# Performance work log

Hardware: AMD Instinct MI355X
Metric: run time of the kernel (lower is better)

Reference implementation:

```python
import jax, jax.numpy as jnp
import numpy as np

EXPR_MASK_RATIO = 0.4
POS_MASK_RATIO = 0.33
MIN_VISIBLE_GENES = 10


def setup_inputs() -> dict:
    key = jax.random.key(0)
    k1, k2 = jax.random.split(key)
    expression = jax.random.normal(k1, (16, 1024, 2000), dtype=jnp.float32)
    position = jax.random.normal(k2, (16, 1024, 3), dtype=jnp.float32)
    return {"expression": expression, "position": position}


def _expression_mask(expression, key):
    # strategy == 'random': rand matrix, kthvalue threshold, mask = rand >= threshold
    B, N, G = expression.shape
    num_masked = max(1, int(G * EXPR_MASK_RATIO))
    num_masked = min(num_masked, G - MIN_VISIBLE_GENES)
    rand = jax.random.uniform(key, (B, N, G), dtype=jnp.float32)
    # torch.kthvalue(rand, G - num_masked): (G - num_masked)-th smallest value,
    # i.e. index G - num_masked - 1 of the ascending sort (keepdim=True).
    kth = jnp.sort(rand, axis=-1)[..., G - num_masked - 1 : G - num_masked]  # (B,N,1)
    return rand >= kth  # bool (B,N,G); includes the threshold element, as in torch code


def _position_mask(position, key):
    # Vectorized form of the per-(b,n) loop:
    #   r < ratio*0.3      -> mask 2 of 3 dims (randperm(3)[:2] == complement of one uniform dim)
    #   ratio*0.3 <= r < ratio -> mask 1 uniform dim
    B, N, _ = position.shape
    kr, k1, k2 = jax.random.split(key, 3)
    r = jax.random.uniform(kr, (B, N), dtype=jnp.float32)
    two = r < POS_MASK_RATIO * 0.3
    one = (r < POS_MASK_RATIO) & (~two)
    dim1 = jax.random.randint(k1, (B, N), 0, 3)  # dim masked in the 1-dim branch
    excl = jax.random.randint(k2, (B, N), 0, 3)  # dim kept in the 2-dim branch
    eye = jnp.eye(3, dtype=bool)
    m1 = eye[dim1]        # (B,N,3) one-hot
    m2 = ~eye[excl]       # (B,N,3) two hot
    false3 = jnp.zeros((B, N, 3), dtype=bool)
    return jnp.where(two[..., None], m2, jnp.where(one[..., None], m1, false3))


def reference(expression, position):
    key = jax.random.key(42)
    ke, kp = jax.random.split(key)
    expr_mask = _expression_mask(expression, ke)   # (B,N,G) bool
    pos_mask = _position_mask(position, kp)        # (B,N,3) bool
    return expr_mask, pos_mask
```

## Files before the change

### kernel.cpp

```cpp
#include <hip/hip_runtime.h>
#include <stdint.h>

#define TF_ROUND(x0, x1, r)                    \
  {                                            \
    x0 += x1;                                  \
    x1 = (x1 << (r)) | (x1 >> (32 - (r)));     \
    x1 ^= x0;                                  \
  }

__host__ __device__ inline void threefry2x32(uint32_t k0, uint32_t k1,
                                             uint32_t x0, uint32_t x1,
                                             uint32_t& o0, uint32_t& o1) {
  const uint32_t ks2 = k0 ^ k1 ^ 0x1BD11BDAu;
  x0 += k0; x1 += k1;
  TF_ROUND(x0, x1, 13) TF_ROUND(x0, x1, 15) TF_ROUND(x0, x1, 26) TF_ROUND(x0, x1, 6)
  x0 += k1; x1 += ks2 + 1u;
  TF_ROUND(x0, x1, 17) TF_ROUND(x0, x1, 29) TF_ROUND(x0, x1, 16) TF_ROUND(x0, x1, 24)
  x0 += ks2; x1 += k0 + 2u;
  TF_ROUND(x0, x1, 13) TF_ROUND(x0, x1, 15) TF_ROUND(x0, x1, 26) TF_ROUND(x0, x1, 6)
  x0 += k0; x1 += k1 + 3u;
  TF_ROUND(x0, x1, 17) TF_ROUND(x0, x1, 29) TF_ROUND(x0, x1, 16) TF_ROUND(x0, x1, 24)
  x0 += k1; x1 += ks2 + 4u;
  TF_ROUND(x0, x1, 13) TF_ROUND(x0, x1, 15) TF_ROUND(x0, x1, 26) TF_ROUND(x0, x1, 6)
  x0 += ks2; x1 += k0 + 5u;
  o0 = x0; o1 = x1;
}

#define RND4(r)                                                     \
  _Pragma("unroll") for (int e = 0; e < 4; ++e) {                   \
    x0[e] += x1[e];                                                 \
    x1[e] = __builtin_amdgcn_alignbit(x1[e], x1[e], 32u - (r));     \
    x1[e] ^= x0[e];                                                 \
  }
#define INJ4(a, b)                                                  \
  _Pragma("unroll") for (int e = 0; e < 4; ++e) {                   \
    x0[e] += (a);                                                   \
    x1[e] += (b);                                                   \
  }

__device__ __forceinline__ void tf4(uint32_t k0, uint32_t k1, uint32_t ks2,
                                    uint32_t tbk, uint32_t lit, uint32_t out[4]) {
  uint32_t x0[4], x1[4];
#pragma unroll
  for (int e = 0; e < 4; ++e) { x0[e] = k0; x1[e] = tbk + (lit + (uint32_t)e); }
  RND4(13) RND4(15) RND4(26) RND4(6)
  INJ4(k1, ks2 + 1u)
  RND4(17) RND4(29) RND4(16) RND4(24)
  INJ4(ks2, k0 + 2u)
  RND4(13) RND4(15) RND4(26) RND4(6)
  INJ4(k0, k1 + 3u)
  RND4(17) RND4(29) RND4(16) RND4(24)
  INJ4(k1, ks2 + 4u)
  RND4(13) RND4(15) RND4(26) RND4(6)
#pragma unroll
  for (int e = 0; e < 4; ++e) out[e] = (x0[e] + ks2) ^ (x1[e] + (k0 + 5u));
}

constexpr int B = 16;
constexpr int N = 1024;
constexpr int G = 2000;
constexpr int NUM_ROWS = B * N;
constexpr uint32_t RANK = (uint32_t)(G - 800 - 1);
constexpr long long EXPR_ELEMS = (long long)NUM_ROWS * G;
constexpr int ROWS_PER_BLOCK = 4;

typedef int v4i __attribute__((ext_vector_type(4)));

__global__ __launch_bounds__(256) void fused_mask_kernel(
    int32_t* __restrict__ out_expr, int32_t* __restrict__ out_pos,
    uint32_t ke0, uint32_t ke1,
    uint32_t kr0, uint32_t kr1,
    uint32_t ah0, uint32_t ah1, uint32_t al0, uint32_t al1,
    uint32_t bh0, uint32_t bh1, uint32_t bl0, uint32_t bl1) {
  __shared__ alignas(16) uint32_t hist[ROWS_PER_BLOCK][256];
  __shared__ uint32_t cand[ROWS_PER_BLOCK][64];
  __shared__ uint32_t cnt[ROWS_PER_BLOCK];

  const int t = threadIdx.x;
  const int lane = t & 63;
  const int w = t >> 6;
  const uint32_t row = blockIdx.x * (uint32_t)ROWS_PER_BLOCK + (uint32_t)w;
  const uint32_t rbase = row * (uint32_t)G;

  {
    uint4 z = make_uint4(0u, 0u, 0u, 0u);
    *reinterpret_cast<uint4*>(&hist[w][lane * 4]) = z;
  }
  if (lane == 0) cnt[w] = 0u;
  __builtin_amdgcn_wave_barrier();

  const uint32_t ks2 = ke0 ^ ke1 ^ 0x1BD11BDAu;
  const uint32_t tbk = rbase + (uint32_t)(lane << 2) + ke1;

  uint32_t m[32];
  uint32_t pb = 0u;

#pragma unroll
  for (int j = 0; j < 7; ++j) {
    uint32_t o[4];
    tf4(ke0, ke1, ks2, tbk, (uint32_t)(j * 256), o);
#pragma unroll
    for (int e = 0; e < 4; ++e) {
      m[j * 4 + e] = o[e] >> 9;
      atomicAdd(&hist[w][o[e] >> 24], 1u);
    }
  }
  if (lane < 52) {
    uint32_t o[4];
    tf4(ke0, ke1, ks2, tbk, 1792u, o);
#pragma unroll
    for (int e = 0; e < 4; ++e) {
      m[28 + e] = o[e] >> 9;
      atomicAdd(&hist[w][o[e] >> 24], 1u);
    }
  } else {
#pragma unroll
    for (int e = 0; e < 4; ++e) m[28 + e] = 0xFFFFFFFFu;
    if (lane < 57) {
      uint32_t pk0, pk1;
      switch (lane) {
        case 52: pk0 = kr0; pk1 = kr1; break;
        case 53: pk0 = ah0; pk1 = ah1; break;
        case 54: pk0 = al0; pk1 = al1; break;
        case 55: pk0 = bh0; pk1 = bh1; break;
        default: pk0 = bl0; pk1 = bl1; break;
      }
      uint32_t y0, y1;
      threefry2x32(pk0, pk1, 0u, row, y0, y1);
      pb = y0 ^ y1;
    }
  }
  __builtin_amdgcn_wave_barrier();

  uint4 h = *reinterpret_cast<const uint4*>(&hist[w][lane * 4]);
  uint32_t tot = h.x + h.y + h.z + h.w;
  uint32_t x = tot;
#pragma unroll
  for (int d = 1; d < 64; d <<= 1) {
    uint32_t o = __shfl_up(x, d, 64);
    if (lane >= d) x += o;
  }
  const uint32_t e0 = x - tot;
  bool found = (e0 <= RANK) && (RANK < x);
  uint32_t bl_ = 0u, kl = 0u;
  if (found) {
    uint32_t e1 = e0 + h.x, e2 = e1 + h.y, e3 = e2 + h.z;
    if (RANK < e1)      { bl_ = 4u * lane + 0u; kl = RANK - e0; }
    else if (RANK < e2) { bl_ = 4u * lane + 1u; kl = RANK - e1; }
    else if (RANK < e3) { bl_ = 4u * lane + 2u; kl = RANK - e2; }
    else                { bl_ = 4u * lane + 3u; kl = RANK - e3; }
  }
  unsigned long long bm = __ballot(found);
  const int src = __builtin_ctzll(bm);
  const uint32_t bucket = (uint32_t)__shfl((int)bl_, src, 64);
  const uint32_t kk = (uint32_t)__shfl((int)kl, src, 64);

#pragma unroll
  for (int i = 0; i < 32; ++i) {
    if ((m[i] >> 15) == bucket) {
      uint32_t p = atomicAdd(&cnt[w], 1u);
      if (p < 64u) cand[w][p] = m[i];
    }
  }
  __builtin_amdgcn_wave_barrier();

  uint32_t c = cnt[w];
  c = (uint32_t)__builtin_amdgcn_readfirstlane((int)c);
  if (c > 64u) c = 64u;
  uint32_t myc = cand[w][lane];
  uint32_t r = 0u;
  for (uint32_t j = 0; j < c; ++j) {
    uint32_t vj = (uint32_t)__shfl((int)myc, (int)j, 64);
    r += (vj < myc || (vj == myc && j < (uint32_t)lane)) ? 1u : 0u;
  }
  bool win = ((uint32_t)lane < c) && (r == kk);
  unsigned long long wm = __ballot(win);
  const uint32_t thr = (uint32_t)__shfl((int)myc, __builtin_ctzll(wm), 64);

  {
    uint32_t p0 = (uint32_t)__shfl((int)pb, 52, 64);
    uint32_t p1 = (uint32_t)__shfl((int)pb, 53, 64);
    uint32_t p2 = (uint32_t)__shfl((int)pb, 54, 64);
    uint32_t p3 = (uint32_t)__shfl((int)pb, 55, 64);
    uint32_t p4 = (uint32_t)__shfl((int)pb, 56, 64);
    if (lane < 3) {
      union { uint32_t u; float f; } cvt;
      cvt.u = (p0 >> 9) | 0x3F800000u;
      float rr = cvt.f - 1.0f;
      const float THR2 = (float)(0.33 * 0.3);
      const float THR1 = (float)0.33;
      bool two = rr < THR2;
      bool one = (rr < THR1) && !two;
      int dim1 = (int)(((p1 % 3u) + (p2 % 3u)) % 3u);
      int excl = (int)(((p3 % 3u) + (p4 % 3u)) % 3u);
      bool mval = two ? (lane != excl) : (one ? (lane == dim1) : false);
      out_pos[row * 3u + (uint32_t)lane] = mval ? 1 : 0;
    }
  }

  int32_t* op = out_expr + rbase + (uint32_t)(lane << 2);
#pragma unroll
  for (int j = 0; j < 7; ++j) {
    v4i a;
    a.x = (m[j * 4 + 0] >= thr) ? 1 : 0;
    a.y = (m[j * 4 + 1] >= thr) ? 1 : 0;
    a.z = (m[j * 4 + 2] >= thr) ? 1 : 0;
    a.w = (m[j * 4 + 3] >= thr) ? 1 : 0;
    __builtin_nontemporal_store(a, (v4i*)(op + j * 256));
  }
  if (lane < 52) {
    v4i a;
    a.x = (m[28] >= thr) ? 1 : 0;
    a.y = (m[29] >= thr) ? 1 : 0;
    a.z = (m[30] >= thr) ? 1 : 0;
    a.w = (m[31] >= thr) ? 1 : 0;
    __builtin_nontemporal_store(a, (v4i*)(op + 1792));
  }
}

extern "C" void kernel_launch(void* const* d_in, const int* in_sizes, int n_in,
                              void* d_out, int out_size, void* d_ws, size_t ws_size,
                              hipStream_t stream) {
  (void)d_in; (void)in_sizes; (void)n_in; (void)d_ws; (void)ws_size; (void)out_size;

  uint32_t ke0, ke1, kp0, kp1;
  threefry2x32(0u, 42u, 0u, 0u, ke0, ke1);
  threefry2x32(0u, 42u, 0u, 1u, kp0, kp1);
  uint32_t kr0, kr1, ka0, ka1, kb0, kb1;
  threefry2x32(kp0, kp1, 0u, 0u, kr0, kr1);
  threefry2x32(kp0, kp1, 0u, 1u, ka0, ka1);
  threefry2x32(kp0, kp1, 0u, 2u, kb0, kb1);
  uint32_t ah0, ah1, al0, al1, bh0, bh1, bl0, bl1;
  threefry2x32(ka0, ka1, 0u, 0u, ah0, ah1);
  threefry2x32(ka0, ka1, 0u, 1u, al0, al1);
  threefry2x32(kb0, kb1, 0u, 0u, bh0, bh1);
  threefry2x32(kb0, kb1, 0u, 1u, bl0, bl1);

  int32_t* out_expr = (int32_t*)d_out;
  int32_t* out_pos = out_expr + EXPR_ELEMS;

  fused_mask_kernel<<<NUM_ROWS / ROWS_PER_BLOCK, 256, 0, stream>>>(
      out_expr, out_pos, ke0, ke1, kr0, kr1,
      ah0, ah1, al0, al1, bh0, bh1, bl0, bl1);
}
```

Before: 244.5 us.

## Replace LDS histogram selection with ballot-based radix bisection for kth threshold

Drops the per-wave 256-bin LDS histogram, its atomics and the prefix scan. The top 7 bits of the threshold are now found by bitwise bisection, counting values below each trial bound with ballot and popcount over all 32 registers per lane. The remaining 16 bits are resolved the same way over the gathered candidates instead of an O(c) pairwise rank loop. The threefry key injection is also folded into the following round to save adds. The coarse stage costs 7 passes of 32 compares plus ballots, which may outweigh the removed LDS atomics.

```diff
diff --git a/kernel.cpp b/kernel.cpp
--- a/kernel.cpp
+++ b/kernel.cpp
@@ -32,28 +32,35 @@
     x1[e] = __builtin_amdgcn_alignbit(x1[e], x1[e], 32u - (r));     \
     x1[e] ^= x0[e];                                                 \
   }
-#define INJ4(a, b)                                                  \
+#define FUSED4(A, Bc, r)                                            \
   _Pragma("unroll") for (int e = 0; e < 4; ++e) {                   \
-    x0[e] += (a);                                                   \
-    x1[e] += (b);                                                   \
+    x1[e] += (Bc);                                                  \
+    x0[e] = x0[e] + (A) + x1[e];                                    \
+    x1[e] = __builtin_amdgcn_alignbit(x1[e], x1[e], 32u - (r));     \
+    x1[e] ^= x0[e];                                                 \
   }
 
 __device__ __forceinline__ void tf4(uint32_t k0, uint32_t k1, uint32_t ks2,
-                                    uint32_t tbk, uint32_t lit, uint32_t out[4]) {
+                                    uint32_t tbk, uint32_t lit, uint32_t* o) {
   uint32_t x0[4], x1[4];
 #pragma unroll
-  for (int e = 0; e < 4; ++e) { x0[e] = k0; x1[e] = tbk + (lit + (uint32_t)e); }
-  RND4(13) RND4(15) RND4(26) RND4(6)
-  INJ4(k1, ks2 + 1u)
-  RND4(17) RND4(29) RND4(16) RND4(24)
-  INJ4(ks2, k0 + 2u)
-  RND4(13) RND4(15) RND4(26) RND4(6)
-  INJ4(k0, k1 + 3u)
-  RND4(17) RND4(29) RND4(16) RND4(24)
-  INJ4(k1, ks2 + 4u)
-  RND4(13) RND4(15) RND4(26) RND4(6)
-#pragma unroll
-  for (int e = 0; e < 4; ++e) out[e] = (x0[e] + ks2) ^ (x1[e] + (k0 + 5u));
+  for (int e = 0; e < 4; ++e) {
+    x1[e] = tbk + (lit + (uint32_t)e);
+    x0[e] = k0 + x1[e];
+    x1[e] = __builtin_amdgcn_alignbit(x1[e], x1[e], 32u - 13u);
+    x1[e] ^= x0[e];
+  }
+  RND4(15) RND4(26) RND4(6)
+  FUSED4(k1, ks2 + 1u, 17)
+  RND4(29) RND4(16) RND4(24)
+  FUSED4(ks2, k0 + 2u, 13)
+  RND4(15) RND4(26) RND4(6)
+  FUSED4(k0, k1 + 3u, 17)
+  RND4(29) RND4(16) RND4(24)
+  FUSED4(k1, ks2 + 4u, 13)
+  RND4(15) RND4(26) RND4(6)
+#pragma unroll
+  for (int e = 0; e < 4; ++e) o[e] = (x0[e] + ks2) ^ (x1[e] + (k0 + 5u));
 }
 
 constexpr int B = 16;
@@ -72,7 +79,6 @@
     uint32_t kr0, uint32_t kr1,
     uint32_t ah0, uint32_t ah1, uint32_t al0, uint32_t al1,
     uint32_t bh0, uint32_t bh1, uint32_t bl0, uint32_t bl1) {
-  __shared__ alignas(16) uint32_t hist[ROWS_PER_BLOCK][256];
   __shared__ uint32_t cand[ROWS_PER_BLOCK][64];
   __shared__ uint32_t cnt[ROWS_PER_BLOCK];
 
@@ -82,40 +88,23 @@
   const uint32_t row = blockIdx.x * (uint32_t)ROWS_PER_BLOCK + (uint32_t)w;
   const uint32_t rbase = row * (uint32_t)G;
 
-  {
-    uint4 z = make_uint4(0u, 0u, 0u, 0u);
-    *reinterpret_cast<uint4*>(&hist[w][lane * 4]) = z;
-  }
   if (lane == 0) cnt[w] = 0u;
-  __builtin_amdgcn_wave_barrier();
 
   const uint32_t ks2 = ke0 ^ ke1 ^ 0x1BD11BDAu;
   const uint32_t tbk = rbase + (uint32_t)(lane << 2) + ke1;
 
-  uint32_t m[32];
+  uint32_t o[32];
   uint32_t pb = 0u;
 
 #pragma unroll
   for (int j = 0; j < 7; ++j) {
-    uint32_t o[4];
-    tf4(ke0, ke1, ks2, tbk, (uint32_t)(j * 256), o);
-#pragma unroll
-    for (int e = 0; e < 4; ++e) {
-      m[j * 4 + e] = o[e] >> 9;
-      atomicAdd(&hist[w][o[e] >> 24], 1u);
-    }
+    tf4(ke0, ke1, ks2, tbk, (uint32_t)(j * 256), &o[j * 4]);
   }
   if (lane < 52) {
-    uint32_t o[4];
-    tf4(ke0, ke1, ks2, tbk, 1792u, o);
-#pragma unroll
-    for (int e = 0; e < 4; ++e) {
-      m[28 + e] = o[e] >> 9;
-      atomicAdd(&hist[w][o[e] >> 24], 1u);
-    }
+    tf4(ke0, ke1, ks2, tbk, 1792u, &o[28]);
   } else {
 #pragma unroll
-    for (int e = 0; e < 4; ++e) m[28 + e] = 0xFFFFFFFFu;
+    for (int e = 0; e < 4; ++e) o[28 + e] = 0xFFFFFFFFu;
     if (lane < 57) {
       uint32_t pk0, pk1;
       switch (lane) {
@@ -130,52 +119,48 @@
       pb = y0 ^ y1;
     }
   }
+
+  uint32_t Bv = 0u, cb = 0u;
+#pragma unroll
+  for (int bit = 6; bit >= 0; --bit) {
+    const uint32_t sthr = (Bv | (1u << bit)) << 25;
+    uint32_t c = 0u;
+#pragma unroll
+    for (int i = 0; i < 32; ++i)
+      c += (uint32_t)__builtin_popcountll(__ballot(o[i] < sthr));
+    if (c <= RANK) { Bv |= (1u << bit); cb = c; }
+  }
+
+#pragma unroll
+  for (int i = 0; i < 28; ++i) {
+    if ((o[i] >> 25) == Bv) {
+      uint32_t p = atomicAdd(&cnt[w], 1u);
+      if (p < 64u) cand[w][p] = o[i] >> 9;
+    }
+  }
+  if (lane < 52) {
+#pragma unroll
+    for (int i = 28; i < 32; ++i) {
+      if ((o[i] >> 25) == Bv) {
+        uint32_t p = atomicAdd(&cnt[w], 1u);
+        if (p < 64u) cand[w][p] = o[i] >> 9;
+      }
+    }
+  }
   __builtin_amdgcn_wave_barrier();
 
-  uint4 h = *reinterpret_cast<const uint4*>(&hist[w][lane * 4]);
-  uint32_t tot = h.x + h.y + h.z + h.w;
-  uint32_t x = tot;
-#pragma unroll
-  for (int d = 1; d < 64; d <<= 1) {
-    uint32_t o = __shfl_up(x, d, 64);
-    if (lane >= d) x += o;
-  }
-  const uint32_t e0 = x - tot;
-  bool found = (e0 <= RANK) && (RANK < x);
-  uint32_t bl_ = 0u, kl = 0u;
-  if (found) {
-    uint32_t e1 = e0 + h.x, e2 = e1 + h.y, e3 = e2 + h.z;
-    if (RANK < e1)      { bl_ = 4u * lane + 0u; kl = RANK - e0; }
-    else if (RANK < e2) { bl_ = 4u * lane + 1u; kl = RANK - e1; }
-    else if (RANK < e3) { bl_ = 4u * lane + 2u; kl = RANK - e2; }
-    else                { bl_ = 4u * lane + 3u; kl = RANK - e3; }
-  }
-  unsigned long long bm = __ballot(found);
-  const int src = __builtin_ctzll(bm);
-  const uint32_t bucket = (uint32_t)__shfl((int)bl_, src, 64);
-  const uint32_t kk = (uint32_t)__shfl((int)kl, src, 64);
-
-#pragma unroll
-  for (int i = 0; i < 32; ++i) {
-    if ((m[i] >> 15) == bucket) {
-      uint32_t p = atomicAdd(&cnt[w], 1u);
-      if (p < 64u) cand[w][p] = m[i];
-    }
-  }
-  __builtin_amdgcn_wave_barrier();
-
   uint32_t c = cnt[w];
-  c = (uint32_t)__builtin_amdgcn_readfirstlane((int)c);
   if (c > 64u) c = 64u;
-  uint32_t myc = cand[w][lane];
-  uint32_t r = 0u;
-  for (uint32_t j = 0; j < c; ++j) {
-    uint32_t vj = (uint32_t)__shfl((int)myc, (int)j, 64);
-    r += (vj < myc || (vj == myc && j < (uint32_t)lane)) ? 1u : 0u;
-  }
-  bool win = ((uint32_t)lane < c) && (r == kk);
-  unsigned long long wm = __ballot(win);
-  const uint32_t thr = (uint32_t)__shfl((int)myc, __builtin_ctzll(wm), 64);
+  const uint32_t myc = ((uint32_t)lane < c) ? cand[w][lane] : 0xFFFFFFFFu;
+  const uint32_t kk = RANK - cb;
+  uint32_t T = Bv << 16;
+#pragma unroll
+  for (int bit = 15; bit >= 0; --bit) {
+    const uint32_t trial = T | (1u << bit);
+    const uint32_t cc = (uint32_t)__builtin_popcountll(__ballot(myc < trial));
+    if (cc <= kk) T = trial;
+  }
+  const uint32_t sT9 = T << 9;
 
   {
     uint32_t p0 = (uint32_t)__shfl((int)pb, 52, 64);
@@ -202,18 +187,18 @@
 #pragma unroll
   for (int j = 0; j < 7; ++j) {
     v4i a;
-    a.x = (m[j * 4 + 0] >= thr) ? 1 : 0;
-    a.y = (m[j * 4 + 1] >= thr) ? 1 : 0;
-    a.z = (m[j * 4 + 2] >= thr) ? 1 : 0;
-    a.w = (m[j * 4 + 3] >= thr) ? 1 : 0;
+    a.x = (o[j * 4 + 0] >= sT9) ? 1 : 0;
+    a.y = (o[j * 4 + 1] >= sT9) ? 1 : 0;
+    a.z = (o[j * 4 + 2] >= sT9) ? 1 : 0;
+    a.w = (o[j * 4 + 3] >= sT9) ? 1 : 0;
     __builtin_nontemporal_store(a, (v4i*)(op + j * 256));
   }
   if (lane < 52) {
     v4i a;
-    a.x = (m[28] >= thr) ? 1 : 0;
-    a.y = (m[29] >= thr) ? 1 : 0;
-    a.z = (m[30] >= thr) ? 1 : 0;
-    a.w = (m[31] >= thr) ? 1 : 0;
+    a.x = (o[28] >= sT9) ? 1 : 0;
+    a.y = (o[29] >= sT9) ? 1 : 0;
+    a.z = (o[30] >= sT9) ? 1 : 0;
+    a.w = (o[31] >= sT9) ? 1 : 0;
     __builtin_nontemporal_store(a, (v4i*)(op + 1792));
   }
 }
```

Result: no change. 247.8 us (+1.3%).
